# Kernel optimization log

Hardware: AMD Instinct MI355X
Metric: run time of the kernel (lower is better)

The kernel has to match this reference:

```python
import jax, jax.numpy as jnp
import numpy as np

NUM_ITERS = 3

def squash(t, axis):
    # scale = |t|^2/(1+|t|^2); out = scale * t / |t|
    sn = jnp.sum(t * t, axis=axis, keepdims=True)
    return (sn / (1.0 + sn)) * t / jnp.sqrt(sn)


def setup_inputs() -> dict:
    key = jax.random.key(0)
    k1, k2, k3, k4 = jax.random.split(key, 4)
    B = 128
    inputs = jax.random.normal(k1, (B, 256, 20, 20), dtype=jnp.float32)
    conv_w = jax.random.normal(k2, (8, 32, 256, 9, 9), dtype=jnp.float32) * 0.05
    conv_b = jax.random.normal(k3, (8, 32), dtype=jnp.float32) * 0.05
    route_weights = jax.random.normal(k4, (10, 1152, 8, 16), dtype=jnp.float32)
    return {"inputs": inputs, "conv_w": conv_w, "conv_b": conv_b,
            "route_weights": route_weights}


def reference(inputs, conv_w, conv_b, route_weights):
    B = inputs.shape[0]
    K, O, Cin, kh, kw = conv_w.shape          # 8 capsules, 32 out-chans each
    # --- primary capsules: 8 parallel convs fused into one grouped-output conv ---
    w = conv_w.reshape(K * O, Cin, kh, kw)
    out = jax.lax.conv_general_dilated(
        inputs, w, window_strides=(2, 2), padding='VALID',
        dimension_numbers=('NCHW', 'OIHW', 'NCHW'))  # [B, K*O, 6, 6]
    out = out + conv_b.reshape(K * O)[None, :, None, None]
    H = out.shape[-1]
    x = out.reshape(B, K, O * H * H).transpose(0, 2, 1)  # [B, 1152, 8]
    x = squash(x, axis=2)
    # --- routing layer ---
    # prediction_vectors: x[None,:,:,None,:] @ W[:,None,:,:,:] -> [10,B,1152,1,16]
    pred = jnp.einsum('bri,crio->cbro', x, route_weights)[:, :, :, None, :]
    logits = jnp.zeros_like(pred)
    v = None
    for i in range(NUM_ITERS):
        # routing_softmax(dim=2): softmax over the routes axis (faithful to source)
        c = jax.nn.softmax(logits, axis=2)
        s = jnp.sum(c * pred, axis=2, keepdims=True)  # [10,B,1,1,16]
        v = squash(s, axis=1)                          # squash default dim=1 (batch) -- faithful
        if i != NUM_ITERS - 1:
            logits = logits + jnp.sum(pred * v, axis=-1, keepdims=True)
    # [10,B,1,1,16] -> squeeze -> [10,B,16] -> permute(1,0,2) -> [B,10,16]
    return jnp.squeeze(v).transpose(1, 0, 2)
```

## Files before the change

### kernel.cpp

```cpp
#include <hip/hip_runtime.h>
#include <math.h>

typedef _Float16 f16;
typedef _Float16 f16x8 __attribute__((ext_vector_type(8)));
typedef float f32x4 __attribute__((ext_vector_type(4)));
typedef float f32x8 __attribute__((ext_vector_type(8)));

#define AS1 __attribute__((address_space(1)))
#define AS3 __attribute__((address_space(3)))

__device__ __forceinline__ void gld_lds16(const f16* g, f16* l) {
#if defined(__has_builtin) && __has_builtin(__builtin_amdgcn_global_load_lds)
    __builtin_amdgcn_global_load_lds((const AS1 void*)g, (AS3 void*)l, 16, 0, 0);
#else
    *(uint4*)l = *(const uint4*)g;
#endif
}

__global__ __launch_bounds__(256) void transpose_input(
    const float* __restrict__ inp, f16* __restrict__ out)
{
    const int b = blockIdx.x, c0 = blockIdx.y * 32, p0 = blockIdx.z * 32;
    const int tx = threadIdx.x, ty = threadIdx.y;
    __shared__ float t[32][33];
#pragma unroll
    for (int j = 0; j < 4; ++j) {
        int c = ty + j * 8, p = p0 + tx;
        if (p < 400) t[c][tx] = inp[((size_t)b * 256 + c0 + c) * 400 + p];
    }
    __syncthreads();
#pragma unroll
    for (int j = 0; j < 4; ++j) {
        int p = p0 + ty + j * 8;
        if (p < 400) out[((size_t)b * 400 + p) * 256 + c0 + tx] = (f16)t[tx][ty + j * 8];
    }
}

__global__ __launch_bounds__(256) void permute_w(
    const float* __restrict__ cw, f16* __restrict__ w_t)
{
    const int n = blockIdx.x, t = threadIdx.x;
    __shared__ f16 buf[81 * 258];
    const float* src = cw + (size_t)n * 20736;
    for (int i = t; i < 20736; i += 256) {
        int cin = i / 81, p = i - cin * 81;
        buf[p * 258 + cin] = (f16)src[i];
    }
    __syncthreads();
    f16* dst = w_t + (size_t)n * 20736;
    for (int j = t; j < 20736; j += 256) {
        int p = j >> 8, cin = j & 255;
        dst[j] = buf[p * 258 + cin];
    }
}

#define SPLITK 14
__global__ __launch_bounds__(256, 2) void conv_mfma(
    const f16* __restrict__ in_t,
    const f16* __restrict__ w_t,
    f16* __restrict__ part)
{
    __shared__ f16 As[3][128 * 32];
    __shared__ f16 Bs[3][256 * 32];
    const int tid = threadIdx.x;
    const int lane = tid & 63, wave = tid >> 6;
    const int wm = wave >> 1, wn = wave & 1;

    const int bid = blockIdx.x + 36 * blockIdx.z;
    const int wgid = (bid & 7) * 63 + (bid >> 3);
    const int m0 = (wgid % 36) * 128;
    const int kz = wgid / 36;

    const int kc0 = kz * 46 + (kz < 4 ? kz : 4);
    const int NT  = (kz < 4) ? 47 : 46;

    int srcA[2], srcB[4];
#pragma unroll
    for (int i = 0; i < 2; ++i) {
        int pairp = i * 32 + (tid >> 3);
        int chunk8 = (tid & 7) ^ (pairp & 7);
        int e = chunk8 >> 2, q4 = chunk8 & 3;
        int m = m0 + pairp * 2 + e;
        int b = m / 36, hw = m - b * 36;
        int ho = hw / 6, wo = hw - ho * 6;
        srcA[i] = ((b * 20 + 2 * ho) * 20 + 2 * wo) * 256 + q4 * 8;
    }
#pragma unroll
    for (int i = 0; i < 4; ++i) {
        int pairp = i * 32 + (tid >> 3);
        int chunk8 = (tid & 7) ^ (pairp & 7);
        int e = chunk8 >> 2, q4 = chunk8 & 3;
        int n = pairp * 2 + e;
        srcB[i] = n * 20736 + q4 * 8;
    }

    const int row = lane & 15, quad = lane >> 4;
    int offA[4], offB[8];
#pragma unroll
    for (int mt = 0; mt < 4; ++mt) {
        int m = wm * 64 + mt * 16 + row;
        int ph8 = (((m & 1) << 2) + quad) ^ ((m >> 1) & 7);
        offA[mt] = (m >> 1) * 64 + ph8 * 8;
    }
#pragma unroll
    for (int nt = 0; nt < 8; ++nt) {
        int n = wn * 128 + nt * 16 + row;
        int ph8 = (((n & 1) << 2) + quad) ^ ((n >> 1) & 7);
        offB[nt] = (n >> 1) * 64 + ph8 * 8;
    }

    f32x4 acc[4][8] = {};

#define KOFFS(T) int kc = kc0 + (T); int pp = kc >> 3, cq = kc & 7;           \
    int kh = pp / 9, kw = pp - kh * 9;                                        \
    int koffA = (kh * 20 + kw) * 256 + cq * 32; int koffB = kc * 32;
#define STAGE1(T, BUF) do { KOFFS(T)                                          \
        gld_lds16(in_t + srcA[0] + koffA, &As[BUF][tid * 8]);                 \
        gld_lds16(in_t + srcA[1] + koffA, &As[BUF][2048 + tid * 8]);          \
        gld_lds16(w_t + srcB[0] + koffB, &Bs[BUF][tid * 8]);                  \
    } while (0)
#define STAGE2(T, BUF) do { KOFFS(T)                                          \
        gld_lds16(w_t + srcB[1] + koffB, &Bs[BUF][2048 + tid * 8]);           \
        gld_lds16(w_t + srcB[2] + koffB, &Bs[BUF][4096 + tid * 8]);           \
        gld_lds16(w_t + srcB[3] + koffB, &Bs[BUF][6144 + tid * 8]);           \
    } while (0)

    STAGE1(0, 0); STAGE2(0, 0);
    STAGE1(1, 1); STAGE2(1, 1);
    asm volatile("s_waitcnt vmcnt(6)" ::: "memory");
    __builtin_amdgcn_s_barrier();

    int buf = 0;
    for (int t = 0; t < NT; ++t) {
        const f16* Ab = &As[buf][0];
        const f16* Bb = &Bs[buf][0];
        int bn = buf + 2; if (bn >= 3) bn -= 3;
        f16x8 af[4], bfr[8];

#pragma unroll
        for (int mt = 0; mt < 4; ++mt) af[mt] = *(const f16x8*)(Ab + offA[mt]);
#pragma unroll
        for (int nt = 0; nt < 4; ++nt) bfr[nt] = *(const f16x8*)(Bb + offB[nt]);
        if (t + 2 < NT) STAGE1(t + 2, bn);
        __builtin_amdgcn_s_barrier();
        asm volatile("s_waitcnt lgkmcnt(0)" ::: "memory");
        __builtin_amdgcn_sched_barrier(0);
        __builtin_amdgcn_s_setprio(1);
#pragma unroll
        for (int mt = 0; mt < 4; ++mt)
#pragma unroll
            for (int nt = 0; nt < 4; ++nt)
                acc[mt][nt] = __builtin_amdgcn_mfma_f32_16x16x32_f16(
                    af[mt], bfr[nt], acc[mt][nt], 0, 0, 0);
        __builtin_amdgcn_s_setprio(0);
        __builtin_amdgcn_s_barrier();

#pragma unroll
        for (int nt = 4; nt < 8; ++nt) bfr[nt] = *(const f16x8*)(Bb + offB[nt]);
        if (t + 2 < NT) STAGE2(t + 2, bn);
        if (t + 2 < NT)
            asm volatile("s_waitcnt vmcnt(6)" ::: "memory");
        else if (t + 1 < NT)
            asm volatile("s_waitcnt vmcnt(0)" ::: "memory");
        __builtin_amdgcn_s_barrier();
        asm volatile("s_waitcnt lgkmcnt(0)" ::: "memory");
        __builtin_amdgcn_sched_barrier(0);
        __builtin_amdgcn_s_setprio(1);
#pragma unroll
        for (int mt = 0; mt < 4; ++mt)
#pragma unroll
            for (int nt = 4; nt < 8; ++nt)
                acc[mt][nt] = __builtin_amdgcn_mfma_f32_16x16x32_f16(
                    af[mt], bfr[nt], acc[mt][nt], 0, 0, 0);
        __builtin_amdgcn_s_setprio(0);
        __builtin_amdgcn_s_barrier();

        if (++buf == 3) buf = 0;
    }
#undef STAGE1
#undef STAGE2
#undef KOFFS

    const int col = lane & 15, qr = (lane >> 4) * 4;
    f16* pb = part + (size_t)kz * 4608 * 256;
#pragma unroll
    for (int mt = 0; mt < 4; ++mt)
#pragma unroll
        for (int rg = 0; rg < 4; ++rg) {
            int m = m0 + wm * 64 + mt * 16 + qr + rg;
#pragma unroll
            for (int nt = 0; nt < 8; ++nt) {
                int n = wn * 128 + nt * 16 + col;
                pb[(size_t)m * 256 + n] = (f16)acc[mt][nt][rg];
            }
        }
}

__global__ __launch_bounds__(256) void combine_squash(
    const f16* __restrict__ part, const float* __restrict__ bias,
    float* __restrict__ x)
{
    int idx = blockIdx.x * 256 + threadIdx.x;
    int m = idx >> 5, o = idx & 31;
    int b = m / 36, hw = m - b * 36;
    float val[8];
#pragma unroll
    for (int k = 0; k < 8; ++k) val[k] = bias[k * 32 + o];
#pragma unroll
    for (int s = 0; s < SPLITK; ++s) {
        const f16* p = part + ((size_t)s * 4608 + m) * 256 + o;
#pragma unroll
        for (int k = 0; k < 8; ++k) val[k] += (float)p[k * 32];
    }
    float sn = 0.f;
#pragma unroll
    for (int k = 0; k < 8; ++k) sn += val[k] * val[k];
    float scale = sqrtf(sn) / (1.f + sn);
    int r = o * 36 + hw;
    float* xp = x + ((size_t)b * 1152 + r) * 8;
#pragma unroll
    for (int k = 0; k < 8; ++k) xp[k] = val[k] * scale;
}

__global__ __launch_bounds__(256) void pred_s0(
    const float* __restrict__ x, const float* __restrict__ rw,
    f16* __restrict__ pred, float* __restrict__ s0)
{
    const int c = blockIdx.x, r0 = blockIdx.y * 32, b0 = blockIdx.z * 32;
    const int tid = threadIdx.x;
    const int o = tid & 15, rp = tid >> 4;
    const int r = r0 + rp * 2;

    __shared__ float s_sh[32 * 16];
    s_sh[tid] = 0.f; s_sh[tid + 256] = 0.f;

    float W0[8], W1[8];
    const float* wb = rw + ((size_t)(c * 1152 + r) * 8) * 16 + o;
#pragma unroll
    for (int k = 0; k < 8; ++k) { W0[k] = wb[k * 16]; W1[k] = wb[128 + k * 16]; }
    __syncthreads();

    for (int bb = 0; bb < 32; ++bb) {
        const int b = b0 + bb;
        const float4* xp = (const float4*)(x + ((size_t)b * 1152 + r) * 8);
        float4 xa = xp[0], xb = xp[1], xc = xp[2], xd = xp[3];
        float p0 = xa.x * W0[0] + xa.y * W0[1] + xa.z * W0[2] + xa.w * W0[3]
                 + xb.x * W0[4] + xb.y * W0[5] + xb.z * W0[6] + xb.w * W0[7];
        float p1 = xc.x * W1[0] + xc.y * W1[1] + xc.z * W1[2] + xc.w * W1[3]
                 + xd.x * W1[4] + xd.y * W1[5] + xd.z * W1[6] + xd.w * W1[7];
        f16* pb = pred + ((size_t)(c * 128 + b) * 1152 + r) * 16 + o;
        pb[0]  = (f16)p0;
        pb[16] = (f16)p1;
        float ps = p0 + p1;
        ps += __shfl_xor(ps, 16);
        ps += __shfl_xor(ps, 32);
        if ((tid & 63) < 16) atomicAdd(&s_sh[bb * 16 + o], ps);
    }
    __syncthreads();
    for (int i = tid; i < 512; i += 256) {
        int bb = i >> 4, oo = i & 15;
        atomicAdd(&s0[((size_t)c * 128 + b0 + bb) * 16 + oo], s_sh[i]);
    }
}

__global__ __launch_bounds__(256) void route_f16(
    const f16* __restrict__ pred, const float* __restrict__ s_in,
    const float* __restrict__ z_in, const float* __restrict__ a_in,
    float* __restrict__ a_out, float* __restrict__ s_out, float* __restrict__ z_out)
{
    const int c = blockIdx.x, b = blockIdx.y, tid = threadIdx.x;
    const size_t base = (size_t)(c * 128 + b) * 1152;

    __shared__ float vs[16];
    __shared__ float mat[128][17];
    __shared__ float red[256][16];
    __shared__ float red2[16][16];
    __shared__ float zred[256];
    __shared__ float zpart[16];

    {
        if (tid < 128) {
            float zin = z_in ? 1.f / z_in[c * 128 + tid] : (1.f / 1152.f);
            const float* sp = s_in + (size_t)(c * 128 + tid) * 16;
#pragma unroll
            for (int o = 0; o < 16; ++o) mat[tid][o] = sp[o] * zin;
        }
        __syncthreads();
        if (tid < 16) {
            float sn = 0.f;
            for (int i = 0; i < 128; ++i) { float q = mat[i][tid]; sn += q * q; }
            vs[tid] = mat[b][tid] * sqrtf(sn) / (1.f + sn);
        }
        __syncthreads();
    }

    float sacc[16];
#pragma unroll
    for (int o = 0; o < 16; ++o) sacc[o] = 0.f;
    float zacc = 0.f;

    for (int r = tid; r < 1152; r += 256) {
        const f16x8* pp = (const f16x8*)(pred + (base + r) * 16);
        f32x8 q0 = __builtin_convertvector(pp[0], f32x8);
        f32x8 q1 = __builtin_convertvector(pp[1], f32x8);
        float contrib = 0.f;
#pragma unroll
        for (int j = 0; j < 8; ++j) contrib += q0[j] * vs[j] + q1[j] * vs[j + 8];
        float an = contrib + (a_in ? a_in[base + r] : 0.f);
        if (a_out) a_out[base + r] = an;
        float e = __expf(an);
#pragma unroll
        for (int j = 0; j < 8; ++j) { sacc[j] += e * q0[j]; sacc[j + 8] += e * q1[j]; }
        zacc += e;
    }

#pragma unroll
    for (int o = 0; o < 16; ++o) red[tid][o] = sacc[o];
    zred[tid] = zacc;
    __syncthreads();
    {
        const int o = tid & 15, seg = tid >> 4;
        float t = 0.f;
#pragma unroll
        for (int j = 0; j < 16; ++j) t += red[seg * 16 + j][o];
        red2[seg][o] = t;
        if (tid < 16) {
            float tz = 0.f;
#pragma unroll
            for (int j = 0; j < 16; ++j) tz += zred[tid * 16 + j];
            zpart[tid] = tz;
        }
    }
    __syncthreads();
    if (tid < 16) {
        float t = 0.f;
#pragma unroll
        for (int seg = 0; seg < 16; ++seg) t += red2[seg][tid];
        s_out[(size_t)(c * 128 + b) * 16 + tid] = t;
    } else if (tid == 16) {
        float tz = 0.f;
#pragma unroll
        for (int j = 0; j < 16; ++j) tz += zpart[j];
        z_out[c * 128 + b] = tz;
    }
}

__global__ __launch_bounds__(128) void squash_final(
    const float* __restrict__ s, const float* __restrict__ z,
    float* __restrict__ out)
{
    const int c = blockIdx.x, b = threadIdx.x;
    float sv[16];
    const float* sp = s + ((size_t)c * 128 + b) * 16;
    float zin = 1.f / z[c * 128 + b];
#pragma unroll
    for (int o = 0; o < 16; ++o) sv[o] = sp[o] * zin;
    __shared__ float m[16][129];
#pragma unroll
    for (int o = 0; o < 16; ++o) m[o][b] = sv[o] * sv[o];
    __syncthreads();
    __shared__ float sn[16];
    if (b < 16) {
        float t = 0.f;
        for (int i = 0; i < 128; ++i) t += m[b][i];
        sn[b] = t;
    }
    __syncthreads();
#pragma unroll
    for (int o = 0; o < 16; ++o) {
        float scale = sqrtf(sn[o]) / (1.f + sn[o]);
        out[((size_t)b * 10 + c) * 16 + o] = sv[o] * scale;
    }
}

extern "C" void kernel_launch(void* const* d_in, const int* in_sizes, int n_in,
                              void* d_out, int out_size, void* d_ws, size_t ws_size,
                              hipStream_t stream)
{
    (void)in_sizes; (void)n_in; (void)out_size; (void)ws_size;
    const float* inp = (const float*)d_in[0];
    const float* cw  = (const float*)d_in[1];
    const float* cb  = (const float*)d_in[2];
    const float* rw  = (const float*)d_in[3];
    float* out = (float*)d_out;

    char* ws = (char*)d_ws;
    f16*   part = (f16*)(ws);
    f16*   pred = (f16*)(ws);
    float* x    = (float*)(ws + 47185920);
    float* a    = (float*)(ws + 51904512);
    float* sA   = (float*)(ws + 57802752);
    float* zA   = (float*)(ws + 57884672);
    float* sB   = (float*)(ws + 57889792);
    float* zB   = (float*)(ws + 57971712);
    f16*   in_t = (f16*)(ws + 57976832);
    f16*   w_t  = (f16*)(ws + 84191232);

    transpose_input<<<dim3(128, 8, 13), dim3(32, 8), 0, stream>>>(inp, in_t);
    permute_w<<<256, 256, 0, stream>>>(cw, w_t);
    conv_mfma<<<dim3(36, 1, SPLITK), 256, 0, stream>>>(in_t, w_t, part);
    combine_squash<<<576, 256, 0, stream>>>(part, cb, x);

    hipMemsetAsync(sA, 0, 81920, stream);
    pred_s0<<<dim3(10, 36, 4), 256, 0, stream>>>(x, rw, pred, sA);

    route_f16<<<dim3(10, 128), 256, 0, stream>>>(pred, sA, nullptr, nullptr,
                                                 a, sB, zB);
    route_f16<<<dim3(10, 128), 256, 0, stream>>>(pred, sB, zB, a,
                                                 nullptr, sA, zA);
    squash_final<<<10, 128, 0, stream>>>(sA, zA, out);
}
```

Measured before the change: 246.1 us.

## Recompute routing predictions on the fly instead of materializing f16 pred tensor

Replaces the pred_s0 kernel and its large f16 prediction tensor with a fused route kernel that recomputes x·W per route inside each routing iteration. Logits are rebuilt as p·(v0+v1) rather than stored and reloaded, and a small v_pre kernel computes the squashed v between passes. The combine_squash kernel is also vectorized to handle four output channels per thread with f16x4 loads and float4 stores. This removes roughly 47 MB of prediction writes and repeated reads, at the cost of extra FMAs and repeated reads of route_weights in each of three passes.

```diff
diff --git a/kernel.cpp b/kernel.cpp
--- a/kernel.cpp
+++ b/kernel.cpp
@@ -2,6 +2,7 @@
 #include <math.h>
 
 typedef _Float16 f16;
+typedef _Float16 f16x4 __attribute__((ext_vector_type(4)));
 typedef _Float16 f16x8 __attribute__((ext_vector_type(8)));
 typedef float f32x4 __attribute__((ext_vector_type(4)));
 typedef float f32x8 __attribute__((ext_vector_type(8)));
@@ -201,147 +202,153 @@
     float* __restrict__ x)
 {
     int idx = blockIdx.x * 256 + threadIdx.x;
-    int m = idx >> 5, o = idx & 31;
+    int m = idx >> 3, g = idx & 7;
     int b = m / 36, hw = m - b * 36;
-    float val[8];
-#pragma unroll
-    for (int k = 0; k < 8; ++k) val[k] = bias[k * 32 + o];
+    float val[8][4];
+#pragma unroll
+    for (int k = 0; k < 8; ++k)
+#pragma unroll
+        for (int j = 0; j < 4; ++j) val[k][j] = bias[k * 32 + g * 4 + j];
 #pragma unroll
     for (int s = 0; s < SPLITK; ++s) {
-        const f16* p = part + ((size_t)s * 4608 + m) * 256 + o;
-#pragma unroll
-        for (int k = 0; k < 8; ++k) val[k] += (float)p[k * 32];
-    }
-    float sn = 0.f;
-#pragma unroll
-    for (int k = 0; k < 8; ++k) sn += val[k] * val[k];
-    float scale = sqrtf(sn) / (1.f + sn);
-    int r = o * 36 + hw;
-    float* xp = x + ((size_t)b * 1152 + r) * 8;
-#pragma unroll
-    for (int k = 0; k < 8; ++k) xp[k] = val[k] * scale;
-}
-
-__global__ __launch_bounds__(256) void pred_s0(
-    const float* __restrict__ x, const float* __restrict__ rw,
-    f16* __restrict__ pred, float* __restrict__ s0)
-{
-    const int c = blockIdx.x, r0 = blockIdx.y * 32, b0 = blockIdx.z * 32;
+        const f16* p = part + ((size_t)s * 4608 + m) * 256 + g * 4;
+#pragma unroll
+        for (int k = 0; k < 8; ++k) {
+            f16x4 v = *(const f16x4*)(p + k * 32);
+#pragma unroll
+            for (int j = 0; j < 4; ++j) val[k][j] += (float)v[j];
+        }
+    }
+#pragma unroll
+    for (int j = 0; j < 4; ++j) {
+        float sn = 0.f;
+#pragma unroll
+        for (int k = 0; k < 8; ++k) sn += val[k][j] * val[k][j];
+        float scale = sqrtf(sn) / (1.f + sn);
+        int r = (g * 4 + j) * 36 + hw;
+        float4* xp = (float4*)(x + ((size_t)b * 1152 + r) * 8);
+        xp[0] = make_float4(val[0][j] * scale, val[1][j] * scale,
+                            val[2][j] * scale, val[3][j] * scale);
+        xp[1] = make_float4(val[4][j] * scale, val[5][j] * scale,
+                            val[6][j] * scale, val[7][j] * scale);
+    }
+}
+
+__global__ __launch_bounds__(256) void route_fused(
+    const float* __restrict__ x,
+    const float* __restrict__ rw,
+    const float* __restrict__ w1,
+    const float* __restrict__ w2,
+    float* __restrict__ s_out,
+    float* __restrict__ z_out)
+{
+    const int c = blockIdx.x, b0 = blockIdx.y * 4;
     const int tid = threadIdx.x;
-    const int o = tid & 15, rp = tid >> 4;
-    const int r = r0 + rp * 2;
-
-    __shared__ float s_sh[32 * 16];
-    s_sh[tid] = 0.f; s_sh[tid + 256] = 0.f;
-
-    float W0[8], W1[8];
-    const float* wb = rw + ((size_t)(c * 1152 + r) * 8) * 16 + o;
-#pragma unroll
-    for (int k = 0; k < 8; ++k) { W0[k] = wb[k * 16]; W1[k] = wb[128 + k * 16]; }
-    __syncthreads();
-
-    for (int bb = 0; bb < 32; ++bb) {
-        const int b = b0 + bb;
-        const float4* xp = (const float4*)(x + ((size_t)b * 1152 + r) * 8);
-        float4 xa = xp[0], xb = xp[1], xc = xp[2], xd = xp[3];
-        float p0 = xa.x * W0[0] + xa.y * W0[1] + xa.z * W0[2] + xa.w * W0[3]
-                 + xb.x * W0[4] + xb.y * W0[5] + xb.z * W0[6] + xb.w * W0[7];
-        float p1 = xc.x * W1[0] + xc.y * W1[1] + xc.z * W1[2] + xc.w * W1[3]
-                 + xd.x * W1[4] + xd.y * W1[5] + xd.z * W1[6] + xd.w * W1[7];
-        f16* pb = pred + ((size_t)(c * 128 + b) * 1152 + r) * 16 + o;
-        pb[0]  = (f16)p0;
-        pb[16] = (f16)p1;
-        float ps = p0 + p1;
-        ps += __shfl_xor(ps, 16);
-        ps += __shfl_xor(ps, 32);
-        if ((tid & 63) < 16) atomicAdd(&s_sh[bb * 16 + o], ps);
-    }
-    __syncthreads();
-    for (int i = tid; i < 512; i += 256) {
-        int bb = i >> 4, oo = i & 15;
-        atomicAdd(&s0[((size_t)c * 128 + b0 + bb) * 16 + oo], s_sh[i]);
-    }
-}
-
-__global__ __launch_bounds__(256) void route_f16(
-    const f16* __restrict__ pred, const float* __restrict__ s_in,
-    const float* __restrict__ z_in, const float* __restrict__ a_in,
-    float* __restrict__ a_out, float* __restrict__ s_out, float* __restrict__ z_out)
-{
-    const int c = blockIdx.x, b = blockIdx.y, tid = threadIdx.x;
-    const size_t base = (size_t)(c * 128 + b) * 1152;
-
-    __shared__ float vs[16];
-    __shared__ float mat[128][17];
-    __shared__ float red[256][16];
-    __shared__ float red2[16][16];
-    __shared__ float zred[256];
-    __shared__ float zpart[16];
-
-    {
-        if (tid < 128) {
-            float zin = z_in ? 1.f / z_in[c * 128 + tid] : (1.f / 1152.f);
-            const float* sp = s_in + (size_t)(c * 128 + tid) * 16;
-#pragma unroll
-            for (int o = 0; o < 16; ++o) mat[tid][o] = sp[o] * zin;
+    const int o = tid & 15, rr = tid >> 4;
+
+    float wv[4] = {0, 0, 0, 0};
+    if (w1) {
+#pragma unroll
+        for (int b = 0; b < 4; ++b) {
+            float t = w1[((size_t)c * 128 + b0 + b) * 16 + o];
+            if (w2) t += w2[((size_t)c * 128 + b0 + b) * 16 + o];
+            wv[b] = t;
+        }
+    }
+
+    __shared__ float xs[4][64][8];
+    float sacc[4] = {0, 0, 0, 0};
+    float zacc[4] = {0, 0, 0, 0};
+
+    for (int R = 0; R < 1152; R += 64) {
+        __syncthreads();
+        {
+            int bb = tid >> 6;
+            int off = (tid & 63) * 8;
+            const float* src = x + ((size_t)(b0 + bb) * 1152 + R) * 8 + off;
+            float4 u0 = ((const float4*)src)[0];
+            float4 u1 = ((const float4*)src)[1];
+            float* d = &xs[bb][0][0] + off;
+            ((float4*)d)[0] = u0; ((float4*)d)[1] = u1;
         }
         __syncthreads();
-        if (tid < 16) {
-            float sn = 0.f;
-            for (int i = 0; i < 128; ++i) { float q = mat[i][tid]; sn += q * q; }
-            vs[tid] = mat[b][tid] * sqrtf(sn) / (1.f + sn);
+#pragma unroll
+        for (int rt = 0; rt < 4; ++rt) {
+            int rl = rt * 16 + rr;
+            int r = R + rl;
+            const float* wp = rw + (((size_t)c * 1152 + r) * 8) * 16 + o;
+            float Wk[8];
+#pragma unroll
+            for (int k = 0; k < 8; ++k) Wk[k] = wp[k * 16];
+#pragma unroll
+            for (int b = 0; b < 4; ++b) {
+                const float* xv = xs[b][rl];
+                float p = xv[0] * Wk[0] + xv[1] * Wk[1] + xv[2] * Wk[2] + xv[3] * Wk[3]
+                        + xv[4] * Wk[4] + xv[5] * Wk[5] + xv[6] * Wk[6] + xv[7] * Wk[7];
+                if (w1) {
+                    float t = p * wv[b];
+                    t += __shfl_xor(t, 1);  t += __shfl_xor(t, 2);
+                    t += __shfl_xor(t, 4);  t += __shfl_xor(t, 8);
+                    float e = __expf(t);
+                    sacc[b] += e * p;
+                    zacc[b] += e;
+                } else {
+                    sacc[b] += p;
+                }
+            }
         }
-        __syncthreads();
-    }
-
-    float sacc[16];
-#pragma unroll
-    for (int o = 0; o < 16; ++o) sacc[o] = 0.f;
-    float zacc = 0.f;
-
-    for (int r = tid; r < 1152; r += 256) {
-        const f16x8* pp = (const f16x8*)(pred + (base + r) * 16);
-        f32x8 q0 = __builtin_convertvector(pp[0], f32x8);
-        f32x8 q1 = __builtin_convertvector(pp[1], f32x8);
-        float contrib = 0.f;
-#pragma unroll
-        for (int j = 0; j < 8; ++j) contrib += q0[j] * vs[j] + q1[j] * vs[j + 8];
-        float an = contrib + (a_in ? a_in[base + r] : 0.f);
-        if (a_out) a_out[base + r] = an;
-        float e = __expf(an);
-#pragma unroll
-        for (int j = 0; j < 8; ++j) { sacc[j] += e * q0[j]; sacc[j + 8] += e * q1[j]; }
-        zacc += e;
-    }
-
-#pragma unroll
-    for (int o = 0; o < 16; ++o) red[tid][o] = sacc[o];
-    zred[tid] = zacc;
-    __syncthreads();
-    {
-        const int o = tid & 15, seg = tid >> 4;
+    }
+
+    __shared__ float red[16][4][16];
+    __shared__ float zr[16][4];
+    __syncthreads();
+#pragma unroll
+    for (int b = 0; b < 4; ++b) red[rr][b][o] = sacc[b];
+    if (o == 0) {
+#pragma unroll
+        for (int b = 0; b < 4; ++b) zr[rr][b] = zacc[b];
+    }
+    __syncthreads();
+    if (tid < 64) {
+        int b = tid >> 4, oo = tid & 15;
         float t = 0.f;
 #pragma unroll
-        for (int j = 0; j < 16; ++j) t += red[seg * 16 + j][o];
-        red2[seg][o] = t;
-        if (tid < 16) {
-            float tz = 0.f;
-#pragma unroll
-            for (int j = 0; j < 16; ++j) tz += zred[tid * 16 + j];
-            zpart[tid] = tz;
-        }
-    }
-    __syncthreads();
-    if (tid < 16) {
+        for (int i = 0; i < 16; ++i) t += red[i][b][oo];
+        s_out[((size_t)c * 128 + b0 + b) * 16 + oo] = t;
+    } else if (z_out && tid < 68) {
+        int b = tid - 64;
         float t = 0.f;
 #pragma unroll
-        for (int seg = 0; seg < 16; ++seg) t += red2[seg][tid];
-        s_out[(size_t)(c * 128 + b) * 16 + tid] = t;
-    } else if (tid == 16) {
-        float tz = 0.f;
-#pragma unroll
-        for (int j = 0; j < 16; ++j) tz += zpart[j];
-        z_out[c * 128 + b] = tz;
+        for (int i = 0; i < 16; ++i) t += zr[i][b];
+        z_out[(size_t)c * 128 + b0 + b] = t;
+    }
+}
+
+__global__ __launch_bounds__(128) void v_pre(
+    const float* __restrict__ s, const float* __restrict__ z,
+    float* __restrict__ v)
+{
+    const int c = blockIdx.x, b = threadIdx.x;
+    float sv[16];
+    const float* sp = s + ((size_t)c * 128 + b) * 16;
+    float zin = z ? 1.f / z[c * 128 + b] : (1.f / 1152.f);
+#pragma unroll
+    for (int o = 0; o < 16; ++o) sv[o] = sp[o] * zin;
+    __shared__ float m[16][129];
+#pragma unroll
+    for (int o = 0; o < 16; ++o) m[o][b] = sv[o] * sv[o];
+    __syncthreads();
+    __shared__ float sn[16];
+    if (b < 16) {
+        float t = 0.f;
+        for (int i = 0; i < 128; ++i) t += m[b][i];
+        sn[b] = t;
+    }
+    __syncthreads();
+#pragma unroll
+    for (int o = 0; o < 16; ++o) {
+        float scale = sqrtf(sn[o]) / (1.f + sn[o]);
+        v[((size_t)c * 128 + b) * 16 + o] = sv[o] * scale;
     }
 }
 
@@ -386,27 +393,25 @@
 
     char* ws = (char*)d_ws;
     f16*   part = (f16*)(ws);
-    f16*   pred = (f16*)(ws);
-    float* x    = (float*)(ws + 47185920);
-    float* a    = (float*)(ws + 51904512);
-    float* sA   = (float*)(ws + 57802752);
-    float* zA   = (float*)(ws + 57884672);
-    float* sB   = (float*)(ws + 57889792);
-    float* zB   = (float*)(ws + 57971712);
-    f16*   in_t = (f16*)(ws + 57976832);
-    f16*   w_t  = (f16*)(ws + 84191232);
+    f16*   in_t = (f16*)(ws + 33030144);
+    f16*   w_t  = (f16*)(ws + 59244544);
+    float* x    = (float*)(ws + 33030144);
+    float* sA   = (float*)(ws + 37748736);
+    float* zA   = (float*)(ws + 37830656);
+    float* sB   = (float*)(ws + 37835776);
+    float* zB   = (float*)(ws + 37917696);
+    float* v0   = (float*)(ws + 37922816);
+    float* v1   = (float*)(ws + 38004736);
 
     transpose_input<<<dim3(128, 8, 13), dim3(32, 8), 0, stream>>>(inp, in_t);
     permute_w<<<256, 256, 0, stream>>>(cw, w_t);
     conv_mfma<<<dim3(36, 1, SPLITK), 256, 0, stream>>>(in_t, w_t, part);
-    combine_squash<<<576, 256, 0, stream>>>(part, cb, x);
-
-    hipMemsetAsync(sA, 0, 81920, stream);
-    pred_s0<<<dim3(10, 36, 4), 256, 0, stream>>>(x, rw, pred, sA);
-
-    route_f16<<<dim3(10, 128), 256, 0, stream>>>(pred, sA, nullptr, nullptr,
-                                                 a, sB, zB);
-    route_f16<<<dim3(10, 128), 256, 0, stream>>>(pred, sB, zB, a,
-                                                 nullptr, sA, zA);
+    combine_squash<<<144, 256, 0, stream>>>(part, cb, x);
+
+    route_fused<<<dim3(10, 32), 256, 0, stream>>>(x, rw, nullptr, nullptr, sA, nullptr);
+    v_pre<<<10, 128, 0, stream>>>(sA, nullptr, v0);
+    route_fused<<<dim3(10, 32), 256, 0, stream>>>(x, rw, v0, nullptr, sB, zB);
+    v_pre<<<10, 128, 0, stream>>>(sB, zB, v1);
+    route_fused<<<dim3(10, 32), 256, 0, stream>>>(x, rw, v0, v1, sA, zA);
     squash_final<<<10, 128, 0, stream>>>(sA, zA, out);
 }
```

Result: slower. 424.5 us (+72.5%).

## Recompute routing logits from summed v vectors; use fp16 x and route weights

Applied to the files above, without the earlier changes.

The routing kernels no longer store and reload a per-route logits array. Because logits are linear in v, the second pass rebuilds the logits from v0+v1, computed from the stored s/z of each iteration. The capsule activations x and the routing weights are now stored in fp16 with vectorized loads and stores, and combine_squash processes four columns per thread. This removes a 5.9MB logits write/read and halves the traffic for x and the weights, at the cost of an extra weight-permute kernel and lower precision on x and W.

```diff
diff --git a/kernel.cpp b/kernel.cpp
--- a/kernel.cpp
+++ b/kernel.cpp
@@ -2,6 +2,7 @@
 #include <math.h>
 
 typedef _Float16 f16;
+typedef _Float16 f16x4 __attribute__((ext_vector_type(4)));
 typedef _Float16 f16x8 __attribute__((ext_vector_type(8)));
 typedef float f32x4 __attribute__((ext_vector_type(4)));
 typedef float f32x8 __attribute__((ext_vector_type(8)));
@@ -52,6 +53,19 @@
         int p = j >> 8, cin = j & 255;
         dst[j] = buf[p * 258 + cin];
     }
+}
+
+__global__ __launch_bounds__(256) void permute_rw(
+    const float* __restrict__ rw, f16* __restrict__ rwh)
+{
+    int g = blockIdx.x * 256 + threadIdx.x;
+    int cr = g >> 5, rem = g & 31;
+    int o = rem >> 1, h = (rem & 1) * 4;
+    const float* src = rw + (size_t)cr * 128 + o;
+    f16x4 v;
+#pragma unroll
+    for (int j = 0; j < 4; ++j) v[j] = (f16)src[(h + j) * 16];
+    *(f16x4*)(rwh + (size_t)cr * 128 + o * 8 + h) = v;
 }
 
 #define SPLITK 14
@@ -198,33 +212,45 @@
 
 __global__ __launch_bounds__(256) void combine_squash(
     const f16* __restrict__ part, const float* __restrict__ bias,
-    float* __restrict__ x)
+    f16* __restrict__ xh)
 {
     int idx = blockIdx.x * 256 + threadIdx.x;
-    int m = idx >> 5, o = idx & 31;
+    int m = idx >> 3, g = idx & 7;
     int b = m / 36, hw = m - b * 36;
-    float val[8];
-#pragma unroll
-    for (int k = 0; k < 8; ++k) val[k] = bias[k * 32 + o];
+    float val[8][4];
+#pragma unroll
+    for (int k = 0; k < 8; ++k)
+#pragma unroll
+        for (int j = 0; j < 4; ++j) val[k][j] = bias[k * 32 + g * 4 + j];
 #pragma unroll
     for (int s = 0; s < SPLITK; ++s) {
-        const f16* p = part + ((size_t)s * 4608 + m) * 256 + o;
-#pragma unroll
-        for (int k = 0; k < 8; ++k) val[k] += (float)p[k * 32];
-    }
-    float sn = 0.f;
-#pragma unroll
-    for (int k = 0; k < 8; ++k) sn += val[k] * val[k];
-    float scale = sqrtf(sn) / (1.f + sn);
-    int r = o * 36 + hw;
-    float* xp = x + ((size_t)b * 1152 + r) * 8;
-#pragma unroll
-    for (int k = 0; k < 8; ++k) xp[k] = val[k] * scale;
-}
-
-__global__ __launch_bounds__(256) void pred_s0(
-    const float* __restrict__ x, const float* __restrict__ rw,
-    f16* __restrict__ pred, float* __restrict__ s0)
+        const f16* p = part + ((size_t)s * 4608 + m) * 256 + g * 4;
+#pragma unroll
+        for (int k = 0; k < 8; ++k) {
+            f16x4 v = *(const f16x4*)(p + k * 32);
+#pragma unroll
+            for (int j = 0; j < 4; ++j) val[k][j] += (float)v[j];
+        }
+    }
+#pragma unroll
+    for (int j = 0; j < 4; ++j) {
+        float sn = 0.f;
+#pragma unroll
+        for (int k = 0; k < 8; ++k) sn += val[k][j] * val[k][j];
+        float scale = sqrtf(sn) / (1.f + sn);
+        int r = (g * 4 + j) * 36 + hw;
+        f16x8 hv;
+#pragma unroll
+        for (int k = 0; k < 8; ++k) hv[k] = (f16)(val[k][j] * scale);
+        *(f16x8*)(xh + ((size_t)b * 1152 + r) * 8) = hv;
+    }
+}
+
+__global__ __launch_bounds__(256) void pred_s0h(
+    const f16* __restrict__ xh,
+    const f16* __restrict__ rwh,
+    f16* __restrict__ pred,
+    float* __restrict__ s0)
 {
     const int c = blockIdx.x, r0 = blockIdx.y * 32, b0 = blockIdx.z * 32;
     const int tid = threadIdx.x;
@@ -234,20 +260,22 @@
     __shared__ float s_sh[32 * 16];
     s_sh[tid] = 0.f; s_sh[tid + 256] = 0.f;
 
-    float W0[8], W1[8];
-    const float* wb = rw + ((size_t)(c * 1152 + r) * 8) * 16 + o;
-#pragma unroll
-    for (int k = 0; k < 8; ++k) { W0[k] = wb[k * 16]; W1[k] = wb[128 + k * 16]; }
+    f16x8 w0h = *(const f16x8*)(rwh + ((size_t)(c * 1152 + r) * 16 + o) * 8);
+    f16x8 w1h = *(const f16x8*)(rwh + ((size_t)(c * 1152 + r + 1) * 16 + o) * 8);
+    f32x8 W0 = __builtin_convertvector(w0h, f32x8);
+    f32x8 W1 = __builtin_convertvector(w1h, f32x8);
     __syncthreads();
 
     for (int bb = 0; bb < 32; ++bb) {
         const int b = b0 + bb;
-        const float4* xp = (const float4*)(x + ((size_t)b * 1152 + r) * 8);
-        float4 xa = xp[0], xb = xp[1], xc = xp[2], xd = xp[3];
-        float p0 = xa.x * W0[0] + xa.y * W0[1] + xa.z * W0[2] + xa.w * W0[3]
-                 + xb.x * W0[4] + xb.y * W0[5] + xb.z * W0[6] + xb.w * W0[7];
-        float p1 = xc.x * W1[0] + xc.y * W1[1] + xc.z * W1[2] + xc.w * W1[3]
-                 + xd.x * W1[4] + xd.y * W1[5] + xd.z * W1[6] + xd.w * W1[7];
+        f16x8 x0h = *(const f16x8*)(xh + ((size_t)b * 1152 + r) * 8);
+        f16x8 x1h = *(const f16x8*)(xh + ((size_t)b * 1152 + r + 1) * 8);
+        f32x8 X0 = __builtin_convertvector(x0h, f32x8);
+        f32x8 X1 = __builtin_convertvector(x1h, f32x8);
+        float p0 = X0[0]*W0[0] + X0[1]*W0[1] + X0[2]*W0[2] + X0[3]*W0[3]
+                 + X0[4]*W0[4] + X0[5]*W0[5] + X0[6]*W0[6] + X0[7]*W0[7];
+        float p1 = X1[0]*W1[0] + X1[1]*W1[1] + X1[2]*W1[2] + X1[3]*W1[3]
+                 + X1[4]*W1[4] + X1[5]*W1[5] + X1[6]*W1[6] + X1[7]*W1[7];
         f16* pb = pred + ((size_t)(c * 128 + b) * 1152 + r) * 16 + o;
         pb[0]  = (f16)p0;
         pb[16] = (f16)p1;
@@ -263,63 +291,79 @@
     }
 }
 
-__global__ __launch_bounds__(256) void route_f16(
-    const f16* __restrict__ pred, const float* __restrict__ s_in,
-    const float* __restrict__ z_in, const float* __restrict__ a_in,
-    float* __restrict__ a_out, float* __restrict__ s_out, float* __restrict__ z_out)
+__global__ __launch_bounds__(256) void route_f16v(
+    const f16* __restrict__ pred,
+    const float* __restrict__ sa, const float* __restrict__ za,
+    const float* __restrict__ sb2, const float* __restrict__ zb2,
+    float* __restrict__ s_out,
+    float* __restrict__ z_out)
 {
     const int c = blockIdx.x, b = blockIdx.y, tid = threadIdx.x;
     const size_t base = (size_t)(c * 128 + b) * 1152;
-
+    const int o = tid & 15, seg = tid >> 4;
+
+    __shared__ float lred[16][17];
     __shared__ float vs[16];
-    __shared__ float mat[128][17];
+
+#define VSADD(S, Z) do {                                                      \
+        float part_ = 0.f;                                                    \
+        _Pragma("unroll")                                                     \
+        for (int j = 0; j < 8; ++j) {                                         \
+            int bb = seg * 8 + j;                                             \
+            float zin = (Z) ? 1.f / (Z)[c * 128 + bb] : (1.f / 1152.f);       \
+            float q = (S)[((size_t)c * 128 + bb) * 16 + o] * zin;             \
+            part_ += q * q;                                                   \
+        }                                                                     \
+        lred[seg][o] = part_;                                                 \
+        __syncthreads();                                                      \
+        if (tid < 16) {                                                       \
+            float t_ = 0.f;                                                   \
+            _Pragma("unroll")                                                 \
+            for (int i = 0; i < 16; ++i) t_ += lred[i][tid];                  \
+            float zin = (Z) ? 1.f / (Z)[c * 128 + b] : (1.f / 1152.f);        \
+            vs[tid] += (S)[((size_t)c * 128 + b) * 16 + tid] * zin *          \
+                       sqrtf(t_) / (1.f + t_);                                \
+        }                                                                     \
+        __syncthreads();                                                      \
+    } while (0)
+
+    if (tid < 16) vs[tid] = 0.f;
+    __syncthreads();
+    VSADD(sa, za);
+    if (sb2) VSADD(sb2, zb2);
+#undef VSADD
+
+    float vr[16];
+#pragma unroll
+    for (int j = 0; j < 16; ++j) vr[j] = vs[j];
+
+    float sacc[16];
+#pragma unroll
+    for (int j = 0; j < 16; ++j) sacc[j] = 0.f;
+    float zacc = 0.f;
+
+    for (int r = tid; r < 1152; r += 256) {
+        const f16x8* pp = (const f16x8*)(pred + (base + r) * 16);
+        f32x8 q0 = __builtin_convertvector(pp[0], f32x8);
+        f32x8 q1 = __builtin_convertvector(pp[1], f32x8);
+        float t = 0.f;
+#pragma unroll
+        for (int j = 0; j < 8; ++j) t += q0[j] * vr[j] + q1[j] * vr[j + 8];
+        float e = __expf(t);
+#pragma unroll
+        for (int j = 0; j < 8; ++j) { sacc[j] += e * q0[j]; sacc[j + 8] += e * q1[j]; }
+        zacc += e;
+    }
+
     __shared__ float red[256][16];
     __shared__ float red2[16][16];
     __shared__ float zred[256];
     __shared__ float zpart[16];
-
+#pragma unroll
+    for (int j = 0; j < 16; ++j) red[tid][j] = sacc[j];
+    zred[tid] = zacc;
+    __syncthreads();
     {
-        if (tid < 128) {
-            float zin = z_in ? 1.f / z_in[c * 128 + tid] : (1.f / 1152.f);
-            const float* sp = s_in + (size_t)(c * 128 + tid) * 16;
-#pragma unroll
-            for (int o = 0; o < 16; ++o) mat[tid][o] = sp[o] * zin;
-        }
-        __syncthreads();
-        if (tid < 16) {
-            float sn = 0.f;
-            for (int i = 0; i < 128; ++i) { float q = mat[i][tid]; sn += q * q; }
-            vs[tid] = mat[b][tid] * sqrtf(sn) / (1.f + sn);
-        }
-        __syncthreads();
-    }
-
-    float sacc[16];
-#pragma unroll
-    for (int o = 0; o < 16; ++o) sacc[o] = 0.f;
-    float zacc = 0.f;
-
-    for (int r = tid; r < 1152; r += 256) {
-        const f16x8* pp = (const f16x8*)(pred + (base + r) * 16);
-        f32x8 q0 = __builtin_convertvector(pp[0], f32x8);
-        f32x8 q1 = __builtin_convertvector(pp[1], f32x8);
-        float contrib = 0.f;
-#pragma unroll
-        for (int j = 0; j < 8; ++j) contrib += q0[j] * vs[j] + q1[j] * vs[j + 8];
-        float an = contrib + (a_in ? a_in[base + r] : 0.f);
-        if (a_out) a_out[base + r] = an;
-        float e = __expf(an);
-#pragma unroll
-        for (int j = 0; j < 8; ++j) { sacc[j] += e * q0[j]; sacc[j + 8] += e * q1[j]; }
-        zacc += e;
-    }
-
-#pragma unroll
-    for (int o = 0; o < 16; ++o) red[tid][o] = sacc[o];
-    zred[tid] = zacc;
-    __syncthreads();
-    {
-        const int o = tid & 15, seg = tid >> 4;
         float t = 0.f;
 #pragma unroll
         for (int j = 0; j < 16; ++j) t += red[seg * 16 + j][o];
@@ -335,7 +379,7 @@
     if (tid < 16) {
         float t = 0.f;
 #pragma unroll
-        for (int seg = 0; seg < 16; ++seg) t += red2[seg][tid];
+        for (int sg = 0; sg < 16; ++sg) t += red2[sg][tid];
         s_out[(size_t)(c * 128 + b) * 16 + tid] = t;
     } else if (tid == 16) {
         float tz = 0.f;
@@ -387,26 +431,29 @@
     char* ws = (char*)d_ws;
     f16*   part = (f16*)(ws);
     f16*   pred = (f16*)(ws);
-    float* x    = (float*)(ws + 47185920);
-    float* a    = (float*)(ws + 51904512);
-    float* sA   = (float*)(ws + 57802752);
-    float* zA   = (float*)(ws + 57884672);
-    float* sB   = (float*)(ws + 57889792);
-    float* zB   = (float*)(ws + 57971712);
-    f16*   in_t = (f16*)(ws + 57976832);
-    f16*   w_t  = (f16*)(ws + 84191232);
+    f16*   in_t = (f16*)(ws + 33030144);
+    f16*   w_t  = (f16*)(ws + 59244544);
+    f16*   rwh  = (f16*)(ws + 69861376);
+    f16*   xh   = (f16*)(ws + 72810496);
+    float* s0   = (float*)(ws + 75169792);
+    float* sB   = (float*)(ws + 75251712);
+    float* sC   = (float*)(ws + 75333632);
+    float* zB   = (float*)(ws + 75415552);
+    float* zC   = (float*)(ws + 75420672);
+
+    hipMemsetAsync(s0, 0, 81920, stream);
 
     transpose_input<<<dim3(128, 8, 13), dim3(32, 8), 0, stream>>>(inp, in_t);
     permute_w<<<256, 256, 0, stream>>>(cw, w_t);
+    permute_rw<<<1440, 256, 0, stream>>>(rw, rwh);
     conv_mfma<<<dim3(36, 1, SPLITK), 256, 0, stream>>>(in_t, w_t, part);
-    combine_squash<<<576, 256, 0, stream>>>(part, cb, x);
-
-    hipMemsetAsync(sA, 0, 81920, stream);
-    pred_s0<<<dim3(10, 36, 4), 256, 0, stream>>>(x, rw, pred, sA);
-
-    route_f16<<<dim3(10, 128), 256, 0, stream>>>(pred, sA, nullptr, nullptr,
-                                                 a, sB, zB);
-    route_f16<<<dim3(10, 128), 256, 0, stream>>>(pred, sB, zB, a,
-                                                 nullptr, sA, zA);
-    squash_final<<<10, 128, 0, stream>>>(sA, zA, out);
-}
+    combine_squash<<<144, 256, 0, stream>>>(part, cb, xh);
+
+    pred_s0h<<<dim3(10, 36, 4), 256, 0, stream>>>(xh, rwh, pred, s0);
+
+    route_f16v<<<dim3(10, 128), 256, 0, stream>>>(pred, s0, nullptr, nullptr, nullptr,
+                                                  sB, zB);
+    route_f16v<<<dim3(10, 128), 256, 0, stream>>>(pred, s0, nullptr, sB, zB,
+                                                  sC, zC);
+    squash_final<<<10, 128, 0, stream>>>(sC, zC, out);
+}
```

Measured after the change: 241.0 us. 2.1% less time.
